# Kernel tuning notes

Hardware: AMD Instinct MI355X
Metric: run time of the kernel (lower is better)

Reference implementation:

```python
import jax, jax.numpy as jnp
import numpy as np

B, T, C = 2, 2048, 1024
H, D = 16, 64


def setup_inputs() -> dict:
    key = jax.random.key(0)
    ks = jax.random.split(key, 5)
    s = 1.0 / np.sqrt(C)  # keep projections well-scaled
    return {
        "x": jax.random.normal(ks[0], (B, T, C), dtype=jnp.float32),
        "wq": jax.random.normal(ks[1], (C, C), dtype=jnp.float32) * s,
        "wk": jax.random.normal(ks[2], (C, C), dtype=jnp.float32) * s,
        "wv": jax.random.normal(ks[3], (C, C), dtype=jnp.float32) * s,
        "wo": jax.random.normal(ks[4], (C, C), dtype=jnp.float32) * s,
    }


def reference(x, wq, wk, wv, wo):
    # nn.Linear(d,d,bias=False): y = x @ W.T ; weights stored [out,in]
    q = (x @ wq.T).reshape(B, T, H, D).transpose(0, 2, 1, 3)  # [B,H,T,D]
    k = (x @ wk.T).reshape(B, T, H, D).transpose(0, 2, 1, 3)
    v = (x @ wv.T).reshape(B, T, H, D).transpose(0, 2, 1, 3)
    scale = jnp.sqrt(jnp.float32(D))
    scores = jnp.einsum("bhtd,bhsd->bhts", q, k) / scale  # [B,H,T,T]
    # additive causal mask: -inf above the diagonal
    causal = jnp.tril(jnp.ones((T, T), dtype=bool))
    scores = jnp.where(causal[None, None], scores, jnp.float32(-1e9))
    weights = jax.nn.softmax(scores, axis=-1)
    out = jnp.einsum("bhts,bhsd->bhtd", weights, v)  # [B,H,T,D]
    out = out.transpose(0, 2, 1, 3).reshape(B, T, C)
    return out @ wo.T
```

## Files before the change

### kernel.cpp

```cpp
#include <hip/hip_runtime.h>
#include <stdint.h>

#define B_ 2
#define T_ 2048
#define C_ 1024
#define H_ 16
#define D_ 64
#define M_ (B_*T_)

typedef __attribute__((ext_vector_type(8))) short bf16x8;
typedef __attribute__((ext_vector_type(4))) short bf16x4;
typedef __attribute__((ext_vector_type(4))) float f32x4;
typedef unsigned short u16;

#define MFMA32(a, b, c) __builtin_amdgcn_mfma_f32_16x16x32_bf16((a), (b), (c), 0, 0, 0)

__device__ __forceinline__ u16 f2bf(float f) {
  union { float f; uint32_t u; } v; v.f = f;
  uint32_t u = v.u;
  return (u16)((u + 0x7fffu + ((u >> 16) & 1u)) >> 16);
}

__device__ __forceinline__ float exp2_fast(float x) { return __builtin_amdgcn_exp2f(x); }

typedef const __attribute__((address_space(1))) void* gas_t;
typedef __attribute__((address_space(3))) void* las_t;
__device__ __forceinline__ void gld_lds16(const void* g, void* l) {
  __builtin_amdgcn_global_load_lds((gas_t)g, (las_t)l, 16, 0, 0);
}

__global__ void cvt_all(const float* __restrict__ x,
                        const float* __restrict__ w0, const float* __restrict__ w1,
                        const float* __restrict__ w2, const float* __restrict__ w3,
                        u16* __restrict__ xb,
                        u16* __restrict__ d0, u16* __restrict__ d1,
                        u16* __restrict__ d2, u16* __restrict__ d3) {
  size_t i = ((size_t)blockIdx.x * 256 + threadIdx.x) * 4;
  const float* s; u16* d; size_t off;
  const size_t NX = (size_t)M_ * C_;
  const size_t NW = (size_t)C_ * C_;
  if (i < NX) { s = x; d = xb; off = i; }
  else {
    size_t j = i - NX;
    int w = (int)(j / NW); off = j - (size_t)w * NW;
    switch (w) {
      case 0: s = w0; d = d0; break;
      case 1: s = w1; d = d1; break;
      case 2: s = w2; d = d2; break;
      default: s = w3; d = d3; break;
    }
  }
  float4 v = *(const float4*)(s + off);
  ushort4 o;
  o.x = f2bf(v.x); o.y = f2bf(v.y); o.z = f2bf(v.z); o.w = f2bf(v.w);
  *(ushort4*)(d + off) = o;
}

__device__ __forceinline__ void gemm_core(const u16* __restrict__ A,
                                          const u16* __restrict__ W,
                                          int m0, int n0, int Kt,
                                          f32x4 acc[4][4])
{
  __shared__ u16 As[128*64];
  __shared__ u16 Bs[128*64];
  const int t = threadIdx.x;
  const int lane = t & 63;
  const int wave = t >> 6;
  const int q = lane >> 4;
  const int l15 = lane & 15;
  const int wm = (wave >> 1) * 64;
  const int wn = (wave & 1) * 64;

  #pragma unroll
  for (int i = 0; i < 4; ++i)
    #pragma unroll
    for (int j = 0; j < 4; ++j)
      acc[i][j] = (f32x4){0.f, 0.f, 0.f, 0.f};

  for (int k0 = 0; k0 < Kt; k0 += 64) {
    #pragma unroll
    for (int r = 0; r < 4; ++r) {
      int Lc = r * 256 + t;
      int row = Lc >> 3;
      int gcc = (Lc & 7) ^ (row & 7);
      gld_lds16(A + (size_t)(m0 + row) * Kt + k0 + gcc * 8, As + Lc * 8);
    }
    #pragma unroll
    for (int r = 0; r < 4; ++r) {
      int Lc = r * 256 + t;
      int row = Lc >> 3;
      int gcc = (Lc & 7) ^ (row & 7);
      gld_lds16(W + (size_t)(n0 + row) * Kt + k0 + gcc * 8, Bs + Lc * 8);
    }
    __syncthreads();

    #pragma unroll
    for (int kk = 0; kk < 2; ++kk) {
      bf16x8 af[4], bfr[4];
      #pragma unroll
      for (int i = 0; i < 4; ++i) {
        int m = wm + i * 16 + l15;
        int ch = (kk * 4 + q) ^ (m & 7);
        af[i] = *(const bf16x8*)(As + m * 64 + ch * 8);
      }
      #pragma unroll
      for (int j = 0; j < 4; ++j) {
        int n = wn + j * 16 + l15;
        int ch = (kk * 4 + q) ^ (n & 7);
        bfr[j] = *(const bf16x8*)(Bs + n * 64 + ch * 8);
      }
      #pragma unroll
      for (int i = 0; i < 4; ++i)
        #pragma unroll
        for (int j = 0; j < 4; ++j)
          acc[i][j] = MFMA32(af[i], bfr[j], acc[i][j]);
    }
    __syncthreads();
  }
}

#define QSCALE 0.1803368801111244f
__global__ __launch_bounds__(256, 3)
void gemm_qkv(const u16* __restrict__ X,
              const u16* __restrict__ Wq, const u16* __restrict__ Wk,
              const u16* __restrict__ Wv,
              u16* __restrict__ Q, u16* __restrict__ K, u16* __restrict__ Vt)
{
  const int bm = blockIdx.x;
  const int bn = blockIdx.y;
  const int seg = bn >> 3;
  const int nb = (bn & 7) * 128;

  const int t = threadIdx.x, lane = t & 63, wave = t >> 6;
  const int q = lane >> 4, l15 = lane & 15;
  const int wm = (wave >> 1) * 64, wn = (wave & 1) * 64;

  f32x4 acc[4][4];

  if (seg < 2) {
    const u16* W = (seg == 0) ? Wq : Wk;
    gemm_core(W, X, nb, bm * 128, C_, acc);
    u16* dst = (seg == 0) ? Q : K;
    const float scale = (seg == 0) ? QSCALE : 1.0f;
    #pragma unroll
    for (int i = 0; i < 4; ++i) {
      #pragma unroll
      for (int j = 0; j < 4; ++j) {
        const int o = nb + wm + i * 16 + q * 4;
        const int h = o >> 6, d = o & 63;
        const int mtok = bm * 128 + wn + j * 16 + l15;
        const int b = mtok >> 11, tt = mtok & (T_ - 1);
        ushort4 pk;
        pk.x = f2bf(acc[i][j][0] * scale); pk.y = f2bf(acc[i][j][1] * scale);
        pk.z = f2bf(acc[i][j][2] * scale); pk.w = f2bf(acc[i][j][3] * scale);
        *(ushort4*)(dst + (((size_t)(b * H_ + h)) * T_ + tt) * D_ + d) = pk;
      }
    }
  } else {
    gemm_core(X, Wv, bm * 128, nb, C_, acc);
    #pragma unroll
    for (int i = 0; i < 4; ++i) {
      #pragma unroll
      for (int j = 0; j < 4; ++j) {
        const int mbase = bm * 128 + wm + i * 16 + q * 4;
        const int b = mbase >> 11, tt = mbase & (T_ - 1);
        const int n = nb + wn + j * 16 + l15;
        const int h = n >> 6, d = n & 63;
        const int ttp = (tt & ~31) | ((tt & 12) << 1) | ((tt & 16) >> 2);
        size_t idx = (((size_t)(b * H_ + h)) * D_ + d) * T_ + ttp;
        ushort4 pk;
        pk.x = f2bf(acc[i][j][0]); pk.y = f2bf(acc[i][j][1]);
        pk.z = f2bf(acc[i][j][2]); pk.w = f2bf(acc[i][j][3]);
        *(ushort4*)(Vt + idx) = pk;
      }
    }
  }
}

__global__ __launch_bounds__(256, 2)
void attn(const u16* __restrict__ Q, const u16* __restrict__ K,
          const u16* __restrict__ Vt, u16* __restrict__ Att)
{
  __shared__ u16 Ks[2][128 * 64];
  __shared__ u16 Vs[2][64 * 128];
  const int t = threadIdx.x;
  const int lane = t & 63, wave = t >> 6;
  const int q = lane >> 4, l15 = lane & 15;
  const int pr = blockIdx.x;
  const int bh = blockIdx.y;
  const int qbA = pr * 64;
  const int qbB = (31 - pr) * 64;
  const u16* Qp = Q + (size_t)bh * T_ * D_;
  const u16* Kp = K + (size_t)bh * T_ * D_;
  const u16* Vp = Vt + (size_t)bh * D_ * T_;

  const int rowA = qbA + 4 * l15 + wave;
  const int rowB = qbB + 4 * l15 + wave;
  const u16* qra = Qp + (size_t)rowA * 64;
  const u16* qrb = Qp + (size_t)rowB * 64;
  const bf16x8 aqA0 = *(const bf16x8*)(qra + q * 8);
  const bf16x8 aqA1 = *(const bf16x8*)(qra + 32 + q * 8);
  const bf16x8 aqB0 = *(const bf16x8*)(qrb + q * 8);
  const bf16x8 aqB1 = *(const bf16x8*)(qrb + 32 + q * 8);

  f32x4 oA[4], oB[4];
  #pragma unroll
  for (int j = 0; j < 4; ++j) {
    oA[j] = (f32x4){0.f, 0.f, 0.f, 0.f};
    oB[j] = (f32x4){0.f, 0.f, 0.f, 0.f};
  }
  float lsA = 0.f, lsB = 0.f;

  auto stage = [&](int kb, int buf) {
    #pragma unroll
    for (int r = 0; r < 4; ++r) {
      int c = r * 256 + t, row = c >> 3, gcc = (c & 7) ^ (row & 7);
      gld_lds16(Kp + (size_t)(kb + row) * 64 + gcc * 8, &Ks[buf][c * 8]);
    }
    #pragma unroll
    for (int r = 0; r < 4; ++r) {
      int c = r * 256 + t, row = c >> 4, gcc = (c & 15) ^ (row & 15);
      gld_lds16(Vp + (size_t)row * T_ + kb + gcc * 8, &Vs[buf][c * 8]);
    }
  };

  stage(0, 0);
  int cur = 0;
  for (int kb = 0; kb <= qbB; kb += 128, cur ^= 1) {
    __syncthreads();
    if (kb + 128 <= qbB) stage(kb + 128, cur ^ 1);
    const u16* Kc = &Ks[cur][0];
    const u16* Vc = &Vs[cur][0];

    #pragma unroll
    for (int s = 0; s < 2; ++s) {
      const int kbase = kb + s * 64;
      if (kbase > qbB) break;

      bf16x8 kf0[4], kf1[4];
      #pragma unroll
      for (int j2 = 0; j2 < 4; ++j2) {
        const int rw = s * 64 + j2 * 16 + l15;
        kf0[j2] = *(const bf16x8*)(Kc + rw * 64 + ((q)     ^ (rw & 7)) * 8);
        kf1[j2] = *(const bf16x8*)(Kc + rw * 64 + ((4 + q) ^ (rw & 7)) * 8);
      }
      bf16x8 vfrag[4][2];
      #pragma unroll
      for (int j = 0; j < 4; ++j) {
        const int rw = j * 16 + l15;
        #pragma unroll
        for (int kk = 0; kk < 2; ++kk) {
          const int cc = ((2 * s + kk) * 4 + q) ^ (rw & 15);
          vfrag[j][kk] = *(const bf16x8*)(Vc + rw * 128 + cc * 8);
        }
      }

      auto tile_compute = [&](const bf16x8 a0, const bf16x8 a1, f32x4* o,
                              float& lsum, int rowg, bool diag) {
        bf16x4 pb[4];
        #pragma unroll
        for (int j2 = 0; j2 < 4; ++j2) {
          f32x4 z = (f32x4){0.f, 0.f, 0.f, 0.f};
          z = MFMA32(kf0[j2], a0, z);
          z = MFMA32(kf1[j2], a1, z);
          if (diag) {
            #pragma unroll
            for (int r = 0; r < 4; ++r) {
              const int key = kbase + j2 * 16 + q * 4 + r;
              if (key > rowg) z[r] = -1e30f;
            }
          }
          float p0 = exp2_fast(z[0]), p1 = exp2_fast(z[1]);
          float p2 = exp2_fast(z[2]), p3 = exp2_fast(z[3]);
          lsum += (p0 + p1) + (p2 + p3);
          pb[j2] = (bf16x4){(short)f2bf(p0), (short)f2bf(p1),
                            (short)f2bf(p2), (short)f2bf(p3)};
        }
        #pragma unroll
        for (int kk = 0; kk < 2; ++kk) {
          const bf16x8 pc = __builtin_shufflevector(pb[2 * kk], pb[2 * kk + 1],
                                                    0, 1, 2, 3, 4, 5, 6, 7);
          #pragma unroll
          for (int j = 0; j < 4; ++j)
            o[j] = MFMA32(vfrag[j][kk], pc, o[j]);
        }
      };

      tile_compute(aqB0, aqB1, oB, lsB, rowB, kbase == qbB);
      if (kbase <= qbA)
        tile_compute(aqA0, aqA1, oA, lsA, rowA, kbase == qbA);
    }
  }

  lsA += __shfl_xor(lsA, 16, 64); lsA += __shfl_xor(lsA, 32, 64);
  lsB += __shfl_xor(lsB, 16, 64); lsB += __shfl_xor(lsB, 32, 64);
  const float invA = __builtin_amdgcn_rcpf(lsA);
  const float invB = __builtin_amdgcn_rcpf(lsB);

  const int b = bh >> 4, h = bh & 15;
  #pragma unroll
  for (int j = 0; j < 4; ++j) {
    ushort4 pa, pbk;
    pa.x = f2bf(oA[j][0] * invA); pa.y = f2bf(oA[j][1] * invA);
    pa.z = f2bf(oA[j][2] * invA); pa.w = f2bf(oA[j][3] * invA);
    pbk.x = f2bf(oB[j][0] * invB); pbk.y = f2bf(oB[j][1] * invB);
    pbk.z = f2bf(oB[j][2] * invB); pbk.w = f2bf(oB[j][3] * invB);
    *(ushort4*)(Att + ((size_t)b * T_ + rowA) * C_ + h * 64 + j * 16 + q * 4) = pa;
    *(ushort4*)(Att + ((size_t)b * T_ + rowB) * C_ + h * 64 + j * 16 + q * 4) = pbk;
  }
}

__global__ __launch_bounds__(256, 2)
void gemm_out(const u16* __restrict__ Att, const u16* __restrict__ Wo,
              float* __restrict__ Out)
{
  __shared__ u16 As[64 * 64];
  __shared__ u16 Bs[128 * 64];
  const int t = threadIdx.x;
  const int lane = t & 63, wave = t >> 6;
  const int q = lane >> 4, l15 = lane & 15;
  const int wm = (wave >> 1) * 32, wn = (wave & 1) * 64;
  const int m0 = blockIdx.x * 64;
  const int n0 = blockIdx.y * 128;

  f32x4 acc[2][4];
  #pragma unroll
  for (int i = 0; i < 2; ++i)
    #pragma unroll
    for (int j = 0; j < 4; ++j)
      acc[i][j] = (f32x4){0.f, 0.f, 0.f, 0.f};

  for (int k0 = 0; k0 < C_; k0 += 64) {
    #pragma unroll
    for (int r = 0; r < 2; ++r) {
      int Lc = r * 256 + t, row = Lc >> 3, gcc = (Lc & 7) ^ (row & 7);
      gld_lds16(Wo + (size_t)(m0 + row) * C_ + k0 + gcc * 8, As + Lc * 8);
    }
    #pragma unroll
    for (int r = 0; r < 4; ++r) {
      int Lc = r * 256 + t, row = Lc >> 3, gcc = (Lc & 7) ^ (row & 7);
      gld_lds16(Att + (size_t)(n0 + row) * C_ + k0 + gcc * 8, Bs + Lc * 8);
    }
    __syncthreads();

    #pragma unroll
    for (int kk = 0; kk < 2; ++kk) {
      bf16x8 af[2], bfr[4];
      #pragma unroll
      for (int i = 0; i < 2; ++i) {
        int m = wm + i * 16 + l15;
        int ch = (kk * 4 + q) ^ (m & 7);
        af[i] = *(const bf16x8*)(As + m * 64 + ch * 8);
      }
      #pragma unroll
      for (int j = 0; j < 4; ++j) {
        int n = wn + j * 16 + l15;
        int ch = (kk * 4 + q) ^ (n & 7);
        bfr[j] = *(const bf16x8*)(Bs + n * 64 + ch * 8);
      }
      #pragma unroll
      for (int i = 0; i < 2; ++i)
        #pragma unroll
        for (int j = 0; j < 4; ++j)
          acc[i][j] = MFMA32(af[i], bfr[j], acc[i][j]);
    }
    __syncthreads();
  }

  #pragma unroll
  for (int i = 0; i < 2; ++i) {
    #pragma unroll
    for (int j = 0; j < 4; ++j) {
      const int o = m0 + wm + i * 16 + q * 4;
      const int tok = n0 + wn + j * 16 + l15;
      float4 st = {acc[i][j][0], acc[i][j][1], acc[i][j][2], acc[i][j][3]};
      *(float4*)(Out + (size_t)tok * C_ + o) = st;
    }
  }
}

extern "C" void kernel_launch(void* const* d_in, const int* in_sizes, int n_in,
                              void* d_out, int out_size, void* d_ws, size_t ws_size,
                              hipStream_t stream) {
  const float* x  = (const float*)d_in[0];
  const float* wq = (const float*)d_in[1];
  const float* wk = (const float*)d_in[2];
  const float* wv = (const float*)d_in[3];
  const float* wo = (const float*)d_in[4];
  float* out = (float*)d_out;

  u16* ws  = (u16*)d_ws;
  u16* xb  = ws;
  u16* wqb = xb  + (size_t)M_ * C_;
  u16* wkb = wqb + (size_t)C_ * C_;
  u16* wvb = wkb + (size_t)C_ * C_;
  u16* wob = wvb + (size_t)C_ * C_;
  u16* Qb  = wob + (size_t)C_ * C_;
  u16* Kb  = Qb  + (size_t)M_ * C_;
  u16* Vtb = Kb  + (size_t)M_ * C_;
  u16* Atb = Vtb + (size_t)M_ * C_;

  cvt_all<<<dim3((M_ * C_ + 4 * C_ * C_) / 1024), 256, 0, stream>>>(
      x, wq, wk, wv, wo, xb, wqb, wkb, wvb, wob);

  gemm_qkv<<<dim3(M_ / 128, 24), 256, 0, stream>>>(xb, wqb, wkb, wvb, Qb, Kb, Vtb);
  attn<<<dim3(16, B_ * H_), 256, 0, stream>>>(Qb, Kb, Vtb, Atb);
  gemm_out<<<dim3(C_ / 64, M_ / 128), 256, 0, stream>>>(Atb, wob, out);
}
```

Baseline: 166.3 us.

## Process four causal query tiles per attention block to reuse staged K/V

Each attention block now handles four 64-row query tiles (pr, 15-pr, 16+pr, 31-pr) instead of two, so every K/V tile staged into shared memory serves up to four query tiles. The grid drops to 256 blocks and launch bounds go to one block per CU so the larger accumulator set fits in registers. The probability-to-bf16 conversion also switches from manual rounding to the native __bf16 cast. The aim is to cut global-to-LDS traffic and sync overhead per unit of work. The cost is lower occupancy and fewer blocks than the CU count, which can leave CUs idle and hide latency less well.

```diff
diff --git a/kernel.cpp b/kernel.cpp
--- a/kernel.cpp
+++ b/kernel.cpp
@@ -10,6 +10,7 @@
 
 typedef __attribute__((ext_vector_type(8))) short bf16x8;
 typedef __attribute__((ext_vector_type(4))) short bf16x4;
+typedef __attribute__((ext_vector_type(4))) __bf16 bf16v4;
 typedef __attribute__((ext_vector_type(4))) float f32x4;
 typedef unsigned short u16;
 
@@ -177,7 +178,7 @@
   }
 }
 
-__global__ __launch_bounds__(256, 2)
+__global__ __launch_bounds__(256, 1)
 void attn(const u16* __restrict__ Q, const u16* __restrict__ K,
           const u16* __restrict__ Vt, u16* __restrict__ Att)
 {
@@ -186,30 +187,34 @@
   const int t = threadIdx.x;
   const int lane = t & 63, wave = t >> 6;
   const int q = lane >> 4, l15 = lane & 15;
-  const int pr = blockIdx.x;
-  const int bh = blockIdx.y;
-  const int qbA = pr * 64;
-  const int qbB = (31 - pr) * 64;
+  const int bh = blockIdx.x;
+  const int pr = blockIdx.y;
+  const int tix0 = pr, tix1 = 15 - pr, tix2 = 16 + pr, tix3 = 31 - pr;
   const u16* Qp = Q + (size_t)bh * T_ * D_;
   const u16* Kp = K + (size_t)bh * T_ * D_;
   const u16* Vp = Vt + (size_t)bh * D_ * T_;
 
-  const int rowA = qbA + 4 * l15 + wave;
-  const int rowB = qbB + 4 * l15 + wave;
-  const u16* qra = Qp + (size_t)rowA * 64;
-  const u16* qrb = Qp + (size_t)rowB * 64;
-  const bf16x8 aqA0 = *(const bf16x8*)(qra + q * 8);
-  const bf16x8 aqA1 = *(const bf16x8*)(qra + 32 + q * 8);
-  const bf16x8 aqB0 = *(const bf16x8*)(qrb + q * 8);
-  const bf16x8 aqB1 = *(const bf16x8*)(qrb + 32 + q * 8);
-
-  f32x4 oA[4], oB[4];
-  #pragma unroll
-  for (int j = 0; j < 4; ++j) {
-    oA[j] = (f32x4){0.f, 0.f, 0.f, 0.f};
-    oB[j] = (f32x4){0.f, 0.f, 0.f, 0.f};
-  }
-  float lsA = 0.f, lsB = 0.f;
+  int rowg[4]; int qb[4];
+  qb[0] = tix0 * 64; qb[1] = tix1 * 64; qb[2] = tix2 * 64; qb[3] = tix3 * 64;
+  bf16x8 aq0[4], aq1[4];
+  #pragma unroll
+  for (int i = 0; i < 4; ++i) {
+    rowg[i] = qb[i] + 4 * l15 + wave;
+    const u16* qr = Qp + (size_t)rowg[i] * 64;
+    aq0[i] = *(const bf16x8*)(qr + q * 8);
+    aq1[i] = *(const bf16x8*)(qr + 32 + q * 8);
+  }
+
+  f32x4 o[4][4];
+  float ls[4];
+  #pragma unroll
+  for (int i = 0; i < 4; ++i) {
+    ls[i] = 0.f;
+    #pragma unroll
+    for (int j = 0; j < 4; ++j) o[i][j] = (f32x4){0.f, 0.f, 0.f, 0.f};
+  }
+
+  const int qb3 = qb[3];
 
   auto stage = [&](int kb, int buf) {
     #pragma unroll
@@ -226,16 +231,16 @@
 
   stage(0, 0);
   int cur = 0;
-  for (int kb = 0; kb <= qbB; kb += 128, cur ^= 1) {
+  for (int kb = 0; kb <= qb3; kb += 128, cur ^= 1) {
     __syncthreads();
-    if (kb + 128 <= qbB) stage(kb + 128, cur ^ 1);
+    if (kb + 128 <= qb3) stage(kb + 128, cur ^ 1);
     const u16* Kc = &Ks[cur][0];
     const u16* Vc = &Vs[cur][0];
 
     #pragma unroll
     for (int s = 0; s < 2; ++s) {
       const int kbase = kb + s * 64;
-      if (kbase > qbB) break;
+      if (kbase > qb3) break;
 
       bf16x8 kf0[4], kf1[4];
       #pragma unroll
@@ -255,26 +260,30 @@
         }
       }
 
-      auto tile_compute = [&](const bf16x8 a0, const bf16x8 a1, f32x4* o,
-                              float& lsum, int rowg, bool diag) {
+      #pragma unroll
+      for (int i = 0; i < 4; ++i) {
+        if (kbase > qb[i]) continue;
+        const bool diag = (kbase == qb[i]);
         bf16x4 pb[4];
         #pragma unroll
         for (int j2 = 0; j2 < 4; ++j2) {
           f32x4 z = (f32x4){0.f, 0.f, 0.f, 0.f};
-          z = MFMA32(kf0[j2], a0, z);
-          z = MFMA32(kf1[j2], a1, z);
+          z = MFMA32(kf0[j2], aq0[i], z);
+          z = MFMA32(kf1[j2], aq1[i], z);
           if (diag) {
             #pragma unroll
             for (int r = 0; r < 4; ++r) {
               const int key = kbase + j2 * 16 + q * 4 + r;
-              if (key > rowg) z[r] = -1e30f;
+              if (key > rowg[i]) z[r] = -1e30f;
             }
           }
           float p0 = exp2_fast(z[0]), p1 = exp2_fast(z[1]);
           float p2 = exp2_fast(z[2]), p3 = exp2_fast(z[3]);
-          lsum += (p0 + p1) + (p2 + p3);
-          pb[j2] = (bf16x4){(short)f2bf(p0), (short)f2bf(p1),
-                            (short)f2bf(p2), (short)f2bf(p3)};
+          ls[i] += (p0 + p1) + (p2 + p3);
+          bf16v4 bv;
+          bv[0] = (__bf16)p0; bv[1] = (__bf16)p1;
+          bv[2] = (__bf16)p2; bv[3] = (__bf16)p3;
+          pb[j2] = __builtin_bit_cast(bf16x4, bv);
         }
         #pragma unroll
         for (int kk = 0; kk < 2; ++kk) {
@@ -282,31 +291,25 @@
                                                     0, 1, 2, 3, 4, 5, 6, 7);
           #pragma unroll
           for (int j = 0; j < 4; ++j)
-            o[j] = MFMA32(vfrag[j][kk], pc, o[j]);
+            o[i][j] = MFMA32(vfrag[j][kk], pc, o[i][j]);
         }
-      };
-
-      tile_compute(aqB0, aqB1, oB, lsB, rowB, kbase == qbB);
-      if (kbase <= qbA)
-        tile_compute(aqA0, aqA1, oA, lsA, rowA, kbase == qbA);
-    }
-  }
-
-  lsA += __shfl_xor(lsA, 16, 64); lsA += __shfl_xor(lsA, 32, 64);
-  lsB += __shfl_xor(lsB, 16, 64); lsB += __shfl_xor(lsB, 32, 64);
-  const float invA = __builtin_amdgcn_rcpf(lsA);
-  const float invB = __builtin_amdgcn_rcpf(lsB);
+      }
+    }
+  }
 
   const int b = bh >> 4, h = bh & 15;
   #pragma unroll
-  for (int j = 0; j < 4; ++j) {
-    ushort4 pa, pbk;
-    pa.x = f2bf(oA[j][0] * invA); pa.y = f2bf(oA[j][1] * invA);
-    pa.z = f2bf(oA[j][2] * invA); pa.w = f2bf(oA[j][3] * invA);
-    pbk.x = f2bf(oB[j][0] * invB); pbk.y = f2bf(oB[j][1] * invB);
-    pbk.z = f2bf(oB[j][2] * invB); pbk.w = f2bf(oB[j][3] * invB);
-    *(ushort4*)(Att + ((size_t)b * T_ + rowA) * C_ + h * 64 + j * 16 + q * 4) = pa;
-    *(ushort4*)(Att + ((size_t)b * T_ + rowB) * C_ + h * 64 + j * 16 + q * 4) = pbk;
+  for (int i = 0; i < 4; ++i) {
+    float l = ls[i];
+    l += __shfl_xor(l, 16, 64); l += __shfl_xor(l, 32, 64);
+    const float inv = __builtin_amdgcn_rcpf(l);
+    #pragma unroll
+    for (int j = 0; j < 4; ++j) {
+      ushort4 pk;
+      pk.x = f2bf(o[i][j][0] * inv); pk.y = f2bf(o[i][j][1] * inv);
+      pk.z = f2bf(o[i][j][2] * inv); pk.w = f2bf(o[i][j][3] * inv);
+      *(ushort4*)(Att + ((size_t)b * T_ + rowg[i]) * C_ + h * 64 + j * 16 + q * 4) = pk;
+    }
   }
 }
 
@@ -404,6 +407,6 @@
       x, wq, wk, wv, wo, xb, wqb, wkb, wvb, wob);
 
   gemm_qkv<<<dim3(M_ / 128, 24), 256, 0, stream>>>(xb, wqb, wkb, wvb, Qb, Kb, Vtb);
-  attn<<<dim3(16, B_ * H_), 256, 0, stream>>>(Qb, Kb, Vtb, Atb);
+  attn<<<dim3(B_ * H_, 8), 256, 0, stream>>>(Qb, Kb, Vtb, Atb);
   gemm_out<<<dim3(C_ / 64, M_ / 128), 256, 0, stream>>>(Atb, wob, out);
 }
```

Result: slower. 171.1 us (+2.9%).

## Share K/V tiles across two wave groups handling four query tiles per block

Applied to the files above, without the earlier changes.

The attention kernel now launches 512-thread blocks in which two groups of four waves each process a pair of causally balanced query tiles. This lets one staged K/V tile in shared memory serve four query tiles instead of two, halving the global-to-LDS traffic per query and the staging work per thread. It also raises wave priority around the MFMA sections and uses native bf16 conversion for the probabilities. In exchange there are fewer, larger blocks (256 instead of 512), and the group with shorter causal ranges idles while the other finishes the longer loop.

```diff
diff --git a/kernel.cpp b/kernel.cpp
--- a/kernel.cpp
+++ b/kernel.cpp
@@ -10,6 +10,7 @@
 
 typedef __attribute__((ext_vector_type(8))) short bf16x8;
 typedef __attribute__((ext_vector_type(4))) short bf16x4;
+typedef __attribute__((ext_vector_type(4))) __bf16 bf16v4;
 typedef __attribute__((ext_vector_type(4))) float f32x4;
 typedef unsigned short u16;
 
@@ -177,7 +178,7 @@
   }
 }
 
-__global__ __launch_bounds__(256, 2)
+__global__ __launch_bounds__(512, 2)
 void attn(const u16* __restrict__ Q, const u16* __restrict__ K,
           const u16* __restrict__ Vt, u16* __restrict__ Att)
 {
@@ -185,19 +186,22 @@
   __shared__ u16 Vs[2][64 * 128];
   const int t = threadIdx.x;
   const int lane = t & 63, wave = t >> 6;
+  const int w4 = wave & 3, wg = wave >> 2;
   const int q = lane >> 4, l15 = lane & 15;
-  const int pr = blockIdx.x;
-  const int bh = blockIdx.y;
-  const int qbA = pr * 64;
-  const int qbB = (31 - pr) * 64;
+  const int bh = blockIdx.x;
+  const int pr = blockIdx.y;
+  const int tixa = wg ? (15 - pr) : pr;
+  const int tixb = wg ? (16 + pr) : (31 - pr);
+  const int qba = tixa * 64, qbb = tixb * 64;
+  const int qb3 = (31 - pr) * 64;
   const u16* Qp = Q + (size_t)bh * T_ * D_;
   const u16* Kp = K + (size_t)bh * T_ * D_;
   const u16* Vp = Vt + (size_t)bh * D_ * T_;
 
-  const int rowA = qbA + 4 * l15 + wave;
-  const int rowB = qbB + 4 * l15 + wave;
-  const u16* qra = Qp + (size_t)rowA * 64;
-  const u16* qrb = Qp + (size_t)rowB * 64;
+  const int rowa = qba + 4 * l15 + w4;
+  const int rowb = qbb + 4 * l15 + w4;
+  const u16* qra = Qp + (size_t)rowa * 64;
+  const u16* qrb = Qp + (size_t)rowb * 64;
   const bf16x8 aqA0 = *(const bf16x8*)(qra + q * 8);
   const bf16x8 aqA1 = *(const bf16x8*)(qra + 32 + q * 8);
   const bf16x8 aqB0 = *(const bf16x8*)(qrb + q * 8);
@@ -213,29 +217,30 @@
 
   auto stage = [&](int kb, int buf) {
     #pragma unroll
-    for (int r = 0; r < 4; ++r) {
-      int c = r * 256 + t, row = c >> 3, gcc = (c & 7) ^ (row & 7);
+    for (int r = 0; r < 2; ++r) {
+      int c = r * 512 + t, row = c >> 3, gcc = (c & 7) ^ (row & 7);
       gld_lds16(Kp + (size_t)(kb + row) * 64 + gcc * 8, &Ks[buf][c * 8]);
     }
     #pragma unroll
-    for (int r = 0; r < 4; ++r) {
-      int c = r * 256 + t, row = c >> 4, gcc = (c & 15) ^ (row & 15);
+    for (int r = 0; r < 2; ++r) {
+      int c = r * 512 + t, row = c >> 4, gcc = (c & 15) ^ (row & 15);
       gld_lds16(Vp + (size_t)row * T_ + kb + gcc * 8, &Vs[buf][c * 8]);
     }
   };
 
   stage(0, 0);
   int cur = 0;
-  for (int kb = 0; kb <= qbB; kb += 128, cur ^= 1) {
+  for (int kb = 0; kb <= qb3; kb += 128, cur ^= 1) {
     __syncthreads();
-    if (kb + 128 <= qbB) stage(kb + 128, cur ^ 1);
+    if (kb + 128 <= qb3) stage(kb + 128, cur ^ 1);
     const u16* Kc = &Ks[cur][0];
     const u16* Vc = &Vs[cur][0];
 
     #pragma unroll
     for (int s = 0; s < 2; ++s) {
       const int kbase = kb + s * 64;
-      if (kbase > qbB) break;
+      if (kbase > qb3) break;
+      if (kbase > qbb) continue;
 
       bf16x8 kf0[4], kf1[4];
       #pragma unroll
@@ -261,8 +266,10 @@
         #pragma unroll
         for (int j2 = 0; j2 < 4; ++j2) {
           f32x4 z = (f32x4){0.f, 0.f, 0.f, 0.f};
+          __builtin_amdgcn_s_setprio(1);
           z = MFMA32(kf0[j2], a0, z);
           z = MFMA32(kf1[j2], a1, z);
+          __builtin_amdgcn_s_setprio(0);
           if (diag) {
             #pragma unroll
             for (int r = 0; r < 4; ++r) {
@@ -273,9 +280,12 @@
           float p0 = exp2_fast(z[0]), p1 = exp2_fast(z[1]);
           float p2 = exp2_fast(z[2]), p3 = exp2_fast(z[3]);
           lsum += (p0 + p1) + (p2 + p3);
-          pb[j2] = (bf16x4){(short)f2bf(p0), (short)f2bf(p1),
-                            (short)f2bf(p2), (short)f2bf(p3)};
+          bf16v4 bv;
+          bv[0] = (__bf16)p0; bv[1] = (__bf16)p1;
+          bv[2] = (__bf16)p2; bv[3] = (__bf16)p3;
+          pb[j2] = __builtin_bit_cast(bf16x4, bv);
         }
+        __builtin_amdgcn_s_setprio(1);
         #pragma unroll
         for (int kk = 0; kk < 2; ++kk) {
           const bf16x8 pc = __builtin_shufflevector(pb[2 * kk], pb[2 * kk + 1],
@@ -284,11 +294,12 @@
           for (int j = 0; j < 4; ++j)
             o[j] = MFMA32(vfrag[j][kk], pc, o[j]);
         }
+        __builtin_amdgcn_s_setprio(0);
       };
 
-      tile_compute(aqB0, aqB1, oB, lsB, rowB, kbase == qbB);
-      if (kbase <= qbA)
-        tile_compute(aqA0, aqA1, oA, lsA, rowA, kbase == qbA);
+      tile_compute(aqB0, aqB1, oB, lsB, rowb, kbase == qbb);
+      if (kbase <= qba)
+        tile_compute(aqA0, aqA1, oA, lsA, rowa, kbase == qba);
     }
   }
 
@@ -305,8 +316,8 @@
     pa.z = f2bf(oA[j][2] * invA); pa.w = f2bf(oA[j][3] * invA);
     pbk.x = f2bf(oB[j][0] * invB); pbk.y = f2bf(oB[j][1] * invB);
     pbk.z = f2bf(oB[j][2] * invB); pbk.w = f2bf(oB[j][3] * invB);
-    *(ushort4*)(Att + ((size_t)b * T_ + rowA) * C_ + h * 64 + j * 16 + q * 4) = pa;
-    *(ushort4*)(Att + ((size_t)b * T_ + rowB) * C_ + h * 64 + j * 16 + q * 4) = pbk;
+    *(ushort4*)(Att + ((size_t)b * T_ + rowa) * C_ + h * 64 + j * 16 + q * 4) = pa;
+    *(ushort4*)(Att + ((size_t)b * T_ + rowb) * C_ + h * 64 + j * 16 + q * 4) = pbk;
   }
 }
 
@@ -404,6 +415,6 @@
       x, wq, wk, wv, wo, xb, wqb, wkb, wvb, wob);
 
   gemm_qkv<<<dim3(M_ / 128, 24), 256, 0, stream>>>(xb, wqb, wkb, wvb, Qb, Kb, Vtb);
-  attn<<<dim3(16, B_ * H_), 256, 0, stream>>>(Qb, Kb, Vtb, Atb);
+  attn<<<dim3(B_ * H_, 8), 512, 0, stream>>>(Qb, Kb, Vtb, Atb);
   gemm_out<<<dim3(C_ / 64, M_ / 128), 256, 0, stream>>>(Atb, wob, out);
 }
```

Result: no change. 164.0 us (-1.4%).
